# Optimization experiments

Hardware: AMD Instinct MI355X
Metric: run time of the kernel (lower is better)

Reference implementation:

```python
import jax, jax.numpy as jnp
import numpy as np

B = 16
N = [20000, 5000, 1250, 313, 79]          # node counts per pooling level (fine -> coarse)
E = [120000, 30000, 7500, 1878, 474]      # ~6 edges per node (triangle mesh)
FILTERS = [3, 32, 32, 64, 64, 64]
K = 6
Z = 64
COND = 2
N_LAYERS = 4


def setup_inputs():
    ks = iter(jax.random.split(jax.random.key(0), 64))
    inp = {}
    inp["x"] = jax.random.normal(next(ks), (B * N[0], FILTERS[0]), jnp.float32)
    inp["label"] = jax.random.normal(next(ks), (B, COND), jnp.float32)
    for i in range(5):
        inp[f"edges{i}"] = jax.random.randint(next(ks), (2, E[i]), 0, N[i])
    for i in range(4):
        inp[f"ds_idx{i}"] = jax.random.randint(next(ks), (N[i + 1],), 0, N[i])
        inp[f"us_idx{i}"] = jax.random.randint(next(ks), (N[i], 3), 0, N[i + 1])
        inp[f"us_w{i}"] = jax.random.uniform(next(ks), (N[i], 3), jnp.float32)
    for i in range(4):
        inp[f"enc_w{i}"] = 0.1 * jax.random.normal(next(ks), (K, FILTERS[i], FILTERS[i + 1]), jnp.float32)
        inp[f"enc_b{i}"] = 0.1 * jax.random.normal(next(ks), (FILTERS[i + 1],), jnp.float32)
    for i in range(5):
        inp[f"dec_w{i}"] = 0.1 * jax.random.normal(next(ks), (K, FILTERS[-i - 1], FILTERS[-i - 2]), jnp.float32)
    for i in range(4):
        inp[f"dec_b{i}"] = 0.1 * jax.random.normal(next(ks), (FILTERS[-i - 2],), jnp.float32)
    lat_in = N[4] * FILTERS[-1]
    inp["enc_mu_w"] = 0.1 * jax.random.normal(next(ks), (lat_in, Z), jnp.float32)
    inp["enc_mu_b"] = jnp.zeros((Z,), jnp.float32)
    inp["enc_lv_w"] = 0.1 * jax.random.normal(next(ks), (lat_in, Z), jnp.float32)
    inp["enc_lv_b"] = jnp.zeros((Z,), jnp.float32)
    inp["dec_lin_w"] = 0.1 * jax.random.normal(next(ks), (Z + COND, lat_in), jnp.float32)
    inp["dec_lin_b"] = jnp.zeros((lat_in,), jnp.float32)
    return inp


def _sym_norm(edges, n):
    # ChebConv_Coma.norm: norm = D^-1/2[row] * w * D^-1/2[col], unit weights
    row, col = edges[0], edges[1]
    deg = jnp.zeros((n,), jnp.float32).at[row].add(1.0)
    dinv = jnp.where(deg > 0, deg ** -0.5, 0.0)
    return dinv[row] * dinv[col]


def _cheb(x, edges, norm, W, b):
    # Chebyshev recursion: Tx_0=x, Tx_1=L~x, Tx_k=2 L~ Tx_{k-1} - Tx_{k-2}
    src, tgt = edges[0], edges[1]

    def prop(h):  # h: [B, Nn, F] -> scatter-sum of norm-weighted source features
        return jnp.zeros_like(h).at[:, tgt].add(h[:, src] * norm[None, :, None])

    Tx0 = x
    out = jnp.einsum('bnf,fg->bng', Tx0, W[0])
    Tx1 = prop(x)
    out = out + jnp.einsum('bnf,fg->bng', Tx1, W[1])
    for k in range(2, W.shape[0]):
        Tx2 = 2.0 * prop(Tx1) - Tx0
        out = out + jnp.einsum('bnf,fg->bng', Tx2, W[k])
        Tx0, Tx1 = Tx1, Tx2
    return out if b is None else out + b


def _forward(x, label, us_ws, enc_ws, enc_bs, dec_ws, dec_bs,
             enc_mu_w, enc_mu_b, enc_lv_w, enc_lv_b, dec_lin_w, dec_lin_b,
             edges, norms, ds_idx, us_idx):
    h = x.reshape(B, N[0], FILTERS[0])
    # encoder
    for i in range(N_LAYERS):
        h = jax.nn.relu(_cheb(h, edges[i], norms[i], enc_ws[i], enc_bs[i]))
        h = h[:, ds_idx[i]]  # binary downsample matrix == row gather
    h = h.reshape(B, N[4] * FILTERS[-1])
    mu = h @ enc_mu_w + enc_mu_b
    logvar = h @ enc_lv_w + enc_lv_b
    # reparameterize (fixed eps for determinism)
    eps = jax.random.normal(jax.random.key(42), mu.shape, mu.dtype)
    z = mu + eps * jnp.exp(0.5 * logvar)
    # decoder
    h = jnp.concatenate([z, label], axis=1)
    h = jax.nn.relu(h @ dec_lin_w + dec_lin_b).reshape(B, N[4], FILTERS[-1])
    for i in range(N_LAYERS):
        lvl = N_LAYERS - 1 - i
        # barycentric upsample: 3 nonzeros per output row
        h = jnp.einsum('rk,brkf->brf', us_ws[lvl], h[:, us_idx[lvl]])
        h = jax.nn.relu(_cheb(h, edges[lvl], norms[lvl], dec_ws[i], dec_bs[i]))
    # faithful quirk of the original: final conv uses A_edge_index[-1] (coarsest graph edges)
    h = _cheb(h, edges[-1], norms[-1], dec_ws[4], None)
    return h.reshape(-1, FILTERS[0]), mu, logvar


def reference(x, label,
              edges0, edges1, edges2, edges3, edges4,
              ds_idx0, ds_idx1, ds_idx2, ds_idx3,
              us_idx0, us_idx1, us_idx2, us_idx3,
              us_w0, us_w1, us_w2, us_w3,
              enc_w0, enc_w1, enc_w2, enc_w3,
              enc_b0, enc_b1, enc_b2, enc_b3,
              dec_w0, dec_w1, dec_w2, dec_w3, dec_w4,
              dec_b0, dec_b1, dec_b2, dec_b3,
              enc_mu_w, enc_mu_b, enc_lv_w, enc_lv_b, dec_lin_w, dec_lin_b):
    edges = [edges0, edges1, edges2, edges3, edges4]
    norms = [_sym_norm(edges[i], N[i]) for i in range(5)]
    return _forward(x, label,
                    [us_w0, us_w1, us_w2, us_w3],
                    [enc_w0, enc_w1, enc_w2, enc_w3],
                    [enc_b0, enc_b1, enc_b2, enc_b3],
                    [dec_w0, dec_w1, dec_w2, dec_w3, dec_w4],
                    [dec_b0, dec_b1, dec_b2, dec_b3],
                    enc_mu_w, enc_mu_b, enc_lv_w, enc_lv_b, dec_lin_w, dec_lin_b,
                    edges, norms,
                    [ds_idx0, ds_idx1, ds_idx2, ds_idx3],
                    [us_idx0, us_idx1, us_idx2, us_idx3])
```

## Files before the change

### kernel.cpp

```cpp
#include <hip/hip_runtime.h>
#include <cstdint>
#include <cstddef>

#define WG 256
#define NB 16


struct IP5 { const int* e[5]; };
struct Ptr3 { const float* p[3]; };


__global__ void k_zero_i(int* __restrict__ p, int n) {
  int i = blockIdx.x * WG + threadIdx.x;
  if (i < n) p[i] = 0;
}

__global__ void k_hist_all(IP5 ep, int* __restrict__ dsrc, int* __restrict__ dtgt) {
  int i = blockIdx.x * WG + threadIdx.x;
  if (i >= 159852) return;
  int l, eo, ee, no, co;
  if (i < 120000)      { l = 0; eo = 0;      ee = 120000; no = 0;     co = 0; }
  else if (i < 150000) { l = 1; eo = 120000; ee = 30000;  no = 20000; co = 20000; }
  else if (i < 157500) { l = 2; eo = 150000; ee = 7500;   no = 25000; co = 25000; }
  else if (i < 159378) { l = 3; eo = 157500; ee = 1878;   no = 26250; co = 26250; }
  else                 { l = 4; eo = 159378; ee = 474;    no = 26563; co = 26563; }
  int e = i - eo;
  const int* E = ep.e[l];
  atomicAdd(&dsrc[no + E[e]], 1);
  atomicAdd(&dtgt[co + E[ee + e]], 1);
}

__global__ void k_scan_all(const int* __restrict__ deg_all, int* __restrict__ rowptr_all,
                           int* __restrict__ cursor_all) {
  static const int Ns[5] = {20000, 5000, 1250, 313, 20000};
  static const int CO[5] = {0, 20000, 25000, 26250, 26563};
  static const int RO[5] = {0, 20001, 25002, 26253, 26567};
  __shared__ int s[WG];
  int l = blockIdx.x;
  int N = Ns[l];
  const int* deg = deg_all + CO[l];
  int* rowptr = rowptr_all + RO[l];
  int* cursor = cursor_all + CO[l];
  int t = threadIdx.x;
  int chunk = (N + WG - 1) / WG;
  int a = t * chunk;
  int b = min(N, a + chunk);
  int sum = 0;
  for (int i = a; i < b; i++) sum += deg[i];
  s[t] = sum;
  __syncthreads();
  for (int off = 1; off < WG; off <<= 1) {
    int v = (t >= off) ? s[t - off] : 0;
    __syncthreads();
    s[t] += v;
    __syncthreads();
  }
  int run = (t == 0) ? 0 : s[t - 1];
  for (int i = a; i < b; i++) {
    rowptr[i] = run;
    cursor[i] = run;
    run += deg[i];
  }
  if (t == 0) rowptr[N] = s[WG - 1];
}


static __device__ __forceinline__ float erfinv_f(float x) {
  float w = -log1pf(-x * x);
  float p;
  if (w < 5.0f) {
    w -= 2.5f;
    p = 2.81022636e-08f;
    p = fmaf(p, w, 3.43273939e-07f);
    p = fmaf(p, w, -3.5233877e-06f);
    p = fmaf(p, w, -4.39150654e-06f);
    p = fmaf(p, w, 0.00021858087f);
    p = fmaf(p, w, -0.00125372503f);
    p = fmaf(p, w, -0.00417768164f);
    p = fmaf(p, w, 0.246640727f);
    p = fmaf(p, w, 1.50140941f);
  } else {
    w = sqrtf(w) - 3.0f;
    p = -0.000200214257f;
    p = fmaf(p, w, 0.000100950558f);
    p = fmaf(p, w, 0.00134934322f);
    p = fmaf(p, w, -0.00367342844f);
    p = fmaf(p, w, 0.00573950773f);
    p = fmaf(p, w, -0.0076224613f);
    p = fmaf(p, w, 0.00943887047f);
    p = fmaf(p, w, 1.00167406f);
    p = fmaf(p, w, 2.83297682f);
  }
  return p * x;
}

static __device__ __forceinline__ float bits_to_normal(unsigned b) {
  float f = __uint_as_float((b >> 9) | 0x3f800000u) - 1.0f;
  const float lo = -0.99999994f;
  float u = f * (1.0f - lo) + lo;
  u = fmaxf(u, lo);
  return 1.41421356f * erfinv_f(u);
}

static __device__ __forceinline__ float eps_val(int i) {
  unsigned x0 = 0u, x1 = (unsigned)i;
  unsigned ks[3] = {0u, 42u, 0u ^ 42u ^ 0x1BD11BDAu};
  x0 += ks[0];
  x1 += ks[1];
  const int R[2][4] = {{13, 15, 26, 6}, {17, 29, 16, 24}};
#pragma unroll
  for (int it = 0; it < 5; it++) {
#pragma unroll
    for (int j = 0; j < 4; j++) {
      x0 += x1;
      int r = R[it & 1][j];
      x1 = (x1 << r) | (x1 >> (32 - r));
      x1 ^= x0;
    }
    x0 += ks[(it + 1) % 3];
    x1 += ks[(it + 2) % 3] + (unsigned)(it + 1);
  }
  return bits_to_normal(x0 ^ x1);
}

__global__ void k_fill_all(IP5 ep, const int* __restrict__ dsrc, int* __restrict__ cursor,
                           int* __restrict__ csrc, float* __restrict__ csw,
                           float* __restrict__ eps, const float* __restrict__ x,
                           float* __restrict__ sxl) {
  int blk = blockIdx.x;
  if (blk < 625) {
    int i = blk * WG + threadIdx.x;
    if (i >= 159852) return;
    int l, eo, ee, no, co, eb;
    if (i < 120000)      { l = 0; eo = 0;      ee = 120000; no = 0;     co = 0;     eb = 0; }
    else if (i < 150000) { l = 1; eo = 120000; ee = 30000;  no = 20000; co = 20000; eb = 120000; }
    else if (i < 157500) { l = 2; eo = 150000; ee = 7500;   no = 25000; co = 25000; eb = 150000; }
    else if (i < 159378) { l = 3; eo = 157500; ee = 1878;   no = 26250; co = 26250; eb = 157500; }
    else                 { l = 4; eo = 159378; ee = 474;    no = 26563; co = 26563; eb = 159378; }
    int e = i - eo;
    const int* E = ep.e[l];
    int s = E[e], t = E[ee + e];
    float da = (float)dsrc[no + s], db = (float)dsrc[no + t];
    float wa = (da > 0.f) ? (1.0f / sqrtf(da)) : 0.f;
    float wb = (db > 0.f) ? (1.0f / sqrtf(db)) : 0.f;
    int pos = atomicAdd(&cursor[co + t], 1);
    csrc[eb + pos] = s;
    csw[eb + pos] = wa * wb;
  } else if (blk < 629) {
    int j = (blk - 625) * WG + threadIdx.x;
    if (j < 1024) eps[j] = eps_val(j);
  } else {
    int j = (blk - 629) * WG + threadIdx.x;
    if (j >= NB * 20000 * 3) return;
    int f = j % 3;
    int b = (j / 3) % NB;
    int n = j / 48;
    sxl[j] = x[((size_t)b * 20000 + n) * 3 + f];
  }
}


#define RFL_I(v) __builtin_amdgcn_readfirstlane(v)
#define RFL_F(v) __int_as_float(__builtin_amdgcn_readfirstlane(__float_as_int(v)))

template <int F>
__global__ __launch_bounds__(WG) void k_propw(const float* __restrict__ in,
                                              float* __restrict__ out,
                                              const float* __restrict__ sub, float scale,
                                              const int* __restrict__ rowptr,
                                              const int* __restrict__ csrc,
                                              const float* __restrict__ csw, int N) {
  constexpr int C4 = F / 16;
  int node = blockIdx.x * 4 + (threadIdx.x >> 6);
  if (node >= N) return;
  int lane = threadIdx.x & 63;
  const float4* in4 = (const float4*)in;
  float4 acc[C4];
#pragma unroll
  for (int u = 0; u < C4; u++) acc[u] = make_float4(0.f, 0.f, 0.f, 0.f);
  int beg = rowptr[node], end = rowptr[node + 1];
  int j = beg;
  for (; j + 3 < end; j += 4) {
    int s0 = RFL_I(csrc[j]);
    int s1 = RFL_I(csrc[j + 1]);
    int s2 = RFL_I(csrc[j + 2]);
    int s3 = RFL_I(csrc[j + 3]);
    float w0 = RFL_F(csw[j]);
    float w1 = RFL_F(csw[j + 1]);
    float w2 = RFL_F(csw[j + 2]);
    float w3 = RFL_F(csw[j + 3]);
    const float4* p0 = in4 + (size_t)s0 * (4 * F) + lane;
    const float4* p1 = in4 + (size_t)s1 * (4 * F) + lane;
    const float4* p2 = in4 + (size_t)s2 * (4 * F) + lane;
    const float4* p3 = in4 + (size_t)s3 * (4 * F) + lane;
    float4 v0[C4], v1[C4], v2[C4], v3[C4];
#pragma unroll
    for (int u = 0; u < C4; u++) v0[u] = p0[u * 64];
#pragma unroll
    for (int u = 0; u < C4; u++) v1[u] = p1[u * 64];
#pragma unroll
    for (int u = 0; u < C4; u++) v2[u] = p2[u * 64];
#pragma unroll
    for (int u = 0; u < C4; u++) v3[u] = p3[u * 64];
#pragma unroll
    for (int u = 0; u < C4; u++) {
      acc[u].x = fmaf(w0, v0[u].x, acc[u].x); acc[u].y = fmaf(w0, v0[u].y, acc[u].y);
      acc[u].z = fmaf(w0, v0[u].z, acc[u].z); acc[u].w = fmaf(w0, v0[u].w, acc[u].w);
      acc[u].x = fmaf(w1, v1[u].x, acc[u].x); acc[u].y = fmaf(w1, v1[u].y, acc[u].y);
      acc[u].z = fmaf(w1, v1[u].z, acc[u].z); acc[u].w = fmaf(w1, v1[u].w, acc[u].w);
      acc[u].x = fmaf(w2, v2[u].x, acc[u].x); acc[u].y = fmaf(w2, v2[u].y, acc[u].y);
      acc[u].z = fmaf(w2, v2[u].z, acc[u].z); acc[u].w = fmaf(w2, v2[u].w, acc[u].w);
      acc[u].x = fmaf(w3, v3[u].x, acc[u].x); acc[u].y = fmaf(w3, v3[u].y, acc[u].y);
      acc[u].z = fmaf(w3, v3[u].z, acc[u].z); acc[u].w = fmaf(w3, v3[u].w, acc[u].w);
    }
  }
  for (; j < end; j++) {
    int s0 = RFL_I(csrc[j]);
    float w0 = RFL_F(csw[j]);
    const float4* p0 = in4 + (size_t)s0 * (4 * F) + lane;
#pragma unroll
    for (int u = 0; u < C4; u++) {
      float4 v0 = p0[u * 64];
      acc[u].x = fmaf(w0, v0.x, acc[u].x); acc[u].y = fmaf(w0, v0.y, acc[u].y);
      acc[u].z = fmaf(w0, v0.z, acc[u].z); acc[u].w = fmaf(w0, v0.w, acc[u].w);
    }
  }
  float4* o4 = (float4*)out + (size_t)node * (4 * F) + lane;
  if (sub) {
    const float4* s4 = (const float4*)sub + (size_t)node * (4 * F) + lane;
#pragma unroll
    for (int u = 0; u < C4; u++) {
      float4 sv = s4[u * 64];
      float4 r;
      r.x = fmaf(scale, acc[u].x, -sv.x); r.y = fmaf(scale, acc[u].y, -sv.y);
      r.z = fmaf(scale, acc[u].z, -sv.z); r.w = fmaf(scale, acc[u].w, -sv.w);
      o4[u * 64] = r;
    }
  } else {
#pragma unroll
    for (int u = 0; u < C4; u++) {
      float4 r;
      r.x = scale * acc[u].x; r.y = scale * acc[u].y;
      r.z = scale * acc[u].z; r.w = scale * acc[u].w;
      o4[u * 64] = r;
    }
  }
}

__global__ __launch_bounds__(WG) void k_propw3(const float* __restrict__ in,
                                               float* __restrict__ out,
                                               const float* __restrict__ sub, float scale,
                                               const int* __restrict__ rowptr,
                                               const int* __restrict__ csrc,
                                               const float* __restrict__ csw, int N) {
  int node = blockIdx.x * 4 + (threadIdx.x >> 6);
  if (node >= N) return;
  int lane = threadIdx.x & 63;
  if (lane >= 48) return;
  float acc = 0.f;
  int beg = rowptr[node], end = rowptr[node + 1];
  for (int j = beg; j < end; j++) {
    int s = RFL_I(csrc[j]);
    float w = RFL_F(csw[j]);
    acc = fmaf(w, in[(size_t)s * 48 + lane], acc);
  }
  float r = scale * acc;
  if (sub) r -= sub[(size_t)node * 48 + lane];
  out[(size_t)node * 48 + lane] = r;
}


template <int F, int G>
__global__ __launch_bounds__(WG) void k_gemm3(Ptr3 txs, const float* __restrict__ W,
                                              const float* __restrict__ bias,
                                              float* __restrict__ out, int rows,
                                              const int* __restrict__ idx,
                                              int accum, int relu) {
  constexpr int CG = G / 4;
  constexpr int RT = WG / CG;
  constexpr int RPB = RT * 4;
  __shared__ float sW[3 * F * G];
  for (int i = threadIdx.x; i < 3 * F * G; i += WG) sW[i] = W[i];
  __syncthreads();
  int cg = threadIdx.x % CG;
  int rt = threadIdx.x / CG;
  int row0 = blockIdx.x * RPB + rt * 4;
  if (row0 >= rows) return;
  size_t src0 = row0;
  if (idx) {
    int node = row0 >> 4, b = row0 & 15;
    src0 = (size_t)idx[node] * 16 + b;
  }
  float* o = out + (size_t)row0 * G + cg * 4;
  float4 acc[4];
  if (accum) {
#pragma unroll
    for (int r = 0; r < 4; r++) acc[r] = *(const float4*)(o + (size_t)r * G);
  } else if (bias) {
    float4 bv = *(const float4*)(bias + cg * 4);
#pragma unroll
    for (int r = 0; r < 4; r++) acc[r] = bv;
  } else {
#pragma unroll
    for (int r = 0; r < 4; r++) acc[r] = make_float4(0.f, 0.f, 0.f, 0.f);
  }
#pragma unroll
  for (int kk = 0; kk < 3; kk++) {
    const float* tb = txs.p[kk] + src0 * F;
    const float* w = sW + kk * F * G + cg * 4;
    if constexpr (F == 3) {
      float4 w0 = *(const float4*)(w + 0 * G);
      float4 w1 = *(const float4*)(w + 1 * G);
      float4 w2 = *(const float4*)(w + 2 * G);
#pragma unroll
      for (int r = 0; r < 4; r++) {
        float x0 = tb[r * 3 + 0], x1 = tb[r * 3 + 1], x2 = tb[r * 3 + 2];
        acc[r].x = fmaf(x0, w0.x, acc[r].x); acc[r].y = fmaf(x0, w0.y, acc[r].y);
        acc[r].z = fmaf(x0, w0.z, acc[r].z); acc[r].w = fmaf(x0, w0.w, acc[r].w);
        acc[r].x = fmaf(x1, w1.x, acc[r].x); acc[r].y = fmaf(x1, w1.y, acc[r].y);
        acc[r].z = fmaf(x1, w1.z, acc[r].z); acc[r].w = fmaf(x1, w1.w, acc[r].w);
        acc[r].x = fmaf(x2, w2.x, acc[r].x); acc[r].y = fmaf(x2, w2.y, acc[r].y);
        acc[r].z = fmaf(x2, w2.z, acc[r].z); acc[r].w = fmaf(x2, w2.w, acc[r].w);
      }
    } else {
#pragma unroll
      for (int fg = 0; fg < F / 4; fg++) {
        float4 xv[4];
#pragma unroll
        for (int r = 0; r < 4; r++) xv[r] = *(const float4*)(tb + (size_t)r * F + 4 * fg);
        float4 w0 = *(const float4*)(w + (4 * fg + 0) * G);
        float4 w1 = *(const float4*)(w + (4 * fg + 1) * G);
        float4 w2 = *(const float4*)(w + (4 * fg + 2) * G);
        float4 w3 = *(const float4*)(w + (4 * fg + 3) * G);
#pragma unroll
        for (int r = 0; r < 4; r++) {
          acc[r].x = fmaf(xv[r].x, w0.x, acc[r].x); acc[r].y = fmaf(xv[r].x, w0.y, acc[r].y);
          acc[r].z = fmaf(xv[r].x, w0.z, acc[r].z); acc[r].w = fmaf(xv[r].x, w0.w, acc[r].w);
          acc[r].x = fmaf(xv[r].y, w1.x, acc[r].x); acc[r].y = fmaf(xv[r].y, w1.y, acc[r].y);
          acc[r].z = fmaf(xv[r].y, w1.z, acc[r].z); acc[r].w = fmaf(xv[r].y, w1.w, acc[r].w);
          acc[r].x = fmaf(xv[r].z, w2.x, acc[r].x); acc[r].y = fmaf(xv[r].z, w2.y, acc[r].y);
          acc[r].z = fmaf(xv[r].z, w2.z, acc[r].z); acc[r].w = fmaf(xv[r].z, w2.w, acc[r].w);
          acc[r].x = fmaf(xv[r].w, w3.x, acc[r].x); acc[r].y = fmaf(xv[r].w, w3.y, acc[r].y);
          acc[r].z = fmaf(xv[r].w, w3.z, acc[r].z); acc[r].w = fmaf(xv[r].w, w3.w, acc[r].w);
        }
      }
    }
  }
  if (relu) {
#pragma unroll
    for (int r = 0; r < 4; r++) {
      acc[r].x = fmaxf(acc[r].x, 0.f); acc[r].y = fmaxf(acc[r].y, 0.f);
      acc[r].z = fmaxf(acc[r].z, 0.f); acc[r].w = fmaxf(acc[r].w, 0.f);
    }
  }
#pragma unroll
  for (int r = 0; r < 4; r++) *(float4*)(o + (size_t)r * G) = acc[r];
}

__global__ __launch_bounds__(WG) void k_gemm3_final(Ptr3 txs, const float* __restrict__ W,
                                                    const float* __restrict__ W4,
                                                    float* __restrict__ out,
                                                    float* __restrict__ dout, int rows) {
  constexpr int F = 32, G = 32;
  constexpr int CG = 8, RT = 32, RPB = 128;
  __shared__ float sW[3 * F * G];
  __shared__ float sWc[96];
  for (int i = threadIdx.x; i < 3 * F * G; i += WG) sW[i] = W[i];
  if (threadIdx.x < 96)
    sWc[threadIdx.x] = W4[threadIdx.x] - W4[192 + threadIdx.x] + W4[384 + threadIdx.x];
  __syncthreads();
  int cg = threadIdx.x % CG;
  int rt = threadIdx.x / CG;
  int row0 = blockIdx.x * RPB + rt * 4;
  float* o = out + (size_t)row0 * G + cg * 4;
  float4 acc[4];
#pragma unroll
  for (int r = 0; r < 4; r++) acc[r] = *(const float4*)(o + (size_t)r * G);
#pragma unroll
  for (int kk = 0; kk < 3; kk++) {
    const float* tb = txs.p[kk] + (size_t)row0 * F;
    const float* w = sW + kk * F * G + cg * 4;
#pragma unroll
    for (int fg = 0; fg < F / 4; fg++) {
      float4 xv[4];
#pragma unroll
      for (int r = 0; r < 4; r++) xv[r] = *(const float4*)(tb + (size_t)r * F + 4 * fg);
      float4 w0 = *(const float4*)(w + (4 * fg + 0) * G);
      float4 w1 = *(const float4*)(w + (4 * fg + 1) * G);
      float4 w2 = *(const float4*)(w + (4 * fg + 2) * G);
      float4 w3 = *(const float4*)(w + (4 * fg + 3) * G);
#pragma unroll
      for (int r = 0; r < 4; r++) {
        acc[r].x = fmaf(xv[r].x, w0.x, acc[r].x); acc[r].y = fmaf(xv[r].x, w0.y, acc[r].y);
        acc[r].z = fmaf(xv[r].x, w0.z, acc[r].z); acc[r].w = fmaf(xv[r].x, w0.w, acc[r].w);
        acc[r].x = fmaf(xv[r].y, w1.x, acc[r].x); acc[r].y = fmaf(xv[r].y, w1.y, acc[r].y);
        acc[r].z = fmaf(xv[r].y, w1.z, acc[r].z); acc[r].w = fmaf(xv[r].y, w1.w, acc[r].w);
        acc[r].x = fmaf(xv[r].z, w2.x, acc[r].x); acc[r].y = fmaf(xv[r].z, w2.y, acc[r].y);
        acc[r].z = fmaf(xv[r].z, w2.z, acc[r].z); acc[r].w = fmaf(xv[r].z, w2.w, acc[r].w);
        acc[r].x = fmaf(xv[r].w, w3.x, acc[r].x); acc[r].y = fmaf(xv[r].w, w3.y, acc[r].y);
        acc[r].z = fmaf(xv[r].w, w3.z, acc[r].z); acc[r].w = fmaf(xv[r].w, w3.w, acc[r].w);
      }
    }
  }
#pragma unroll
  for (int r = 0; r < 4; r++) {
    acc[r].x = fmaxf(acc[r].x, 0.f); acc[r].y = fmaxf(acc[r].y, 0.f);
    acc[r].z = fmaxf(acc[r].z, 0.f); acc[r].w = fmaxf(acc[r].w, 0.f);
  }
  if ((row0 >> 4) < 79) {
#pragma unroll
    for (int r = 0; r < 4; r++) *(float4*)(o + (size_t)r * G) = acc[r];
  }
#pragma unroll
  for (int r = 0; r < 4; r++) {
    float av[4] = {acc[r].x, acc[r].y, acc[r].z, acc[r].w};
    float p0 = 0.f, p1 = 0.f, p2 = 0.f;
#pragma unroll
    for (int j = 0; j < 4; j++) {
      int f = cg * 4 + j;
      p0 = fmaf(av[j], sWc[f * 3 + 0], p0);
      p1 = fmaf(av[j], sWc[f * 3 + 1], p1);
      p2 = fmaf(av[j], sWc[f * 3 + 2], p2);
    }
#pragma unroll
    for (int m = 4; m >= 1; m >>= 1) {
      p0 += __shfl_xor(p0, m, 64);
      p1 += __shfl_xor(p1, m, 64);
      p2 += __shfl_xor(p2, m, 64);
    }
    if (cg == 0) {
      int row = row0 + r;
      int n = row >> 4, b = row & 15;
      float* od = dout + ((size_t)b * 20000 + n) * 3;
      od[0] = p0; od[1] = p1; od[2] = p2;
    }
  }
}

__global__ __launch_bounds__(256) void k_final_fix(const float* __restrict__ in,
                                                   const float* __restrict__ W,
                                                   const int* __restrict__ rowptr,
                                                   const int* __restrict__ csrc,
                                                   const float* __restrict__ csw,
                                                   float* __restrict__ out) {
  __shared__ float B0[79 * 32], B1[79 * 32], B2[79 * 32];
  __shared__ float sacc[79 * 3];
  __shared__ float sW[576];
  int b = blockIdx.x, t = threadIdx.x;
  for (int i = t; i < 576; i += 256) sW[i] = W[i];
  for (int i = t; i < 2528; i += 256) {
    int r = i >> 5, f = i & 31;
    B0[i] = in[((size_t)r * 16 + b) * 32 + f];
  }
  __syncthreads();
  for (int i = t; i < 237; i += 256) {
    int r = i / 3, g = i % 3;
    float a = 0.f;
    for (int f = 0; f < 32; f++) a = fmaf(B0[r * 32 + f], sW[f * 3 + g], a);
    sacc[i] = a;
  }
  for (int i = t; i < 2528; i += 256) {
    int r = i >> 5, f = i & 31;
    float a = 0.f;
    for (int j = rowptr[r]; j < rowptr[r + 1]; j++) a = fmaf(csw[j], B0[csrc[j] * 32 + f], a);
    B1[i] = a;
  }
  __syncthreads();
  for (int i = t; i < 237; i += 256) {
    int r = i / 3, g = i % 3;
    float a = sacc[i];
    for (int f = 0; f < 32; f++) a = fmaf(B1[r * 32 + f], sW[96 + f * 3 + g], a);
    sacc[i] = a;
  }
  for (int i = t; i < 2528; i += 256) {
    int r = i >> 5, f = i & 31;
    float a = 0.f;
    for (int j = rowptr[r]; j < rowptr[r + 1]; j++) a = fmaf(csw[j], B1[csrc[j] * 32 + f], a);
    B2[i] = 2.f * a - B0[i];
  }
  __syncthreads();
  for (int i = t; i < 237; i += 256) {
    int r = i / 3, g = i % 3;
    float a = sacc[i];
    for (int f = 0; f < 32; f++) a = fmaf(B2[r * 32 + f], sW[192 + f * 3 + g], a);
    sacc[i] = a;
  }
  __syncthreads();
  for (int i = t; i < 2528; i += 256) {
    int r = i >> 5, f = i & 31;
    float a = 0.f;
    for (int j = rowptr[r]; j < rowptr[r + 1]; j++) a = fmaf(csw[j], B2[csrc[j] * 32 + f], a);
    B0[i] = 2.f * a - B1[i];
  }
  __syncthreads();
  for (int i = t; i < 237; i += 256) {
    int r = i / 3, g = i % 3;
    float a = sacc[i];
    for (int f = 0; f < 32; f++) a = fmaf(B0[r * 32 + f], sW[288 + f * 3 + g], a);
    sacc[i] = a;
  }
  __syncthreads();
  for (int i = t; i < 2528; i += 256) {
    int r = i >> 5, f = i & 31;
    float a = 0.f;
    for (int j = rowptr[r]; j < rowptr[r + 1]; j++) a = fmaf(csw[j], B0[csrc[j] * 32 + f], a);
    B1[i] = 2.f * a - B2[i];
  }
  __syncthreads();
  for (int i = t; i < 237; i += 256) {
    int r = i / 3, g = i % 3;
    float a = sacc[i];
    for (int f = 0; f < 32; f++) a = fmaf(B1[r * 32 + f], sW[384 + f * 3 + g], a);
    sacc[i] = a;
  }
  __syncthreads();
  for (int i = t; i < 2528; i += 256) {
    int r = i >> 5, f = i & 31;
    float a = 0.f;
    for (int j = rowptr[r]; j < rowptr[r + 1]; j++) a = fmaf(csw[j], B1[csrc[j] * 32 + f], a);
    B2[i] = 2.f * a - B0[i];
  }
  __syncthreads();
  for (int i = t; i < 237; i += 256) {
    int r = i / 3, g = i % 3;
    float a = sacc[i];
    for (int f = 0; f < 32; f++) a = fmaf(B2[r * 32 + f], sW[480 + f * 3 + g], a);
    out[((size_t)b * 20000 + r) * 3 + g] = a;
  }
}

template <int F>
__global__ __launch_bounds__(WG) void k_us(const float* __restrict__ in,
                                           float* __restrict__ out,
                                           const int* __restrict__ uidx,
                                           const float* __restrict__ uw, int Nf) {
  int i = blockIdx.x * WG + threadIdx.x;
  int total = Nf * NB * F;
  if (i >= total) return;
  int pos = i % (NB * F);
  int r = i / (NB * F);
  float acc = 0.f;
#pragma unroll
  for (int k = 0; k < 3; k++) {
    float v = in[(size_t)uidx[r * 3 + k] * NB * F + pos];
    acc = fmaf(uw[r * 3 + k], fmaxf(v, 0.f), acc);
  }
  out[i] = acc;
}


__global__ __launch_bounds__(64) void k_latent(const float* __restrict__ h,
                                               const float* __restrict__ muW,
                                               const float* __restrict__ muB,
                                               const float* __restrict__ lvW,
                                               const float* __restrict__ lvB,
                                               const float* __restrict__ eps,
                                               const float* __restrict__ label,
                                               float* __restrict__ mu_out,
                                               float* __restrict__ lv_out,
                                               float* __restrict__ hcat) {
  int b = blockIdx.x / 64;
  int g = blockIdx.x % 64;
  int l = threadIdx.x;
  float am = 0.f, al = 0.f;
  for (int i = l; i < 5056; i += 64) {
    int n = i >> 6, f = i & 63;
    float hv = h[(size_t)(n * 16 + b) * 64 + f];
    am = fmaf(hv, muW[(size_t)i * 64 + g], am);
    al = fmaf(hv, lvW[(size_t)i * 64 + g], al);
  }
  for (int off = 32; off > 0; off >>= 1) {
    am += __shfl_down(am, off, 64);
    al += __shfl_down(al, off, 64);
  }
  if (l == 0) {
    am += muB[g];
    al += lvB[g];
    mu_out[b * 64 + g] = am;
    lv_out[b * 64 + g] = al;
    hcat[b * 66 + g] = fmaf(eps[b * 64 + g], expf(0.5f * al), am);
    if (g < 2) hcat[b * 66 + 64 + g] = label[b * 2 + g];
  }
}

__global__ __launch_bounds__(WG) void k_declin(const float* __restrict__ hcat,
                                               const float* __restrict__ W,
                                               const float* __restrict__ bias,
                                               float* __restrict__ out) {
  int idx = blockIdx.x * WG + threadIdx.x;
  if (idx >= NB * 5056) return;
  int b = idx / 5056, j = idx % 5056;
  int n = j >> 6, f = j & 63;
  float acc = bias[j];
  const float* hc = hcat + b * 66;
#pragma unroll
  for (int i = 0; i < 66; i++) acc = fmaf(hc[i], W[(size_t)i * 5056 + j], acc);
  out[(size_t)(n * 16 + b) * 64 + f] = fmaxf(acc, 0.f);
}


static inline dim3 grid1(long n) { return dim3((unsigned)((n + WG - 1) / WG)); }

template <int F, int G>
static void run_cheb(float* in, float* out, float* A, float* B,
                     const float* W, const float* bias, int N, int Nout,
                     const int* ds_idx, int relu_last,
                     const int* rowptr, const int* csrc, const float* csw,
                     hipStream_t st) {
  int orows = NB * Nout;
  constexpr int RPB = (WG / (G / 4)) * 4;
  dim3 gG((unsigned)((orows + RPB - 1) / RPB));
  dim3 gP((unsigned)((N + 3) / 4));
  int relu2 = ds_idx ? 1 : relu_last;
  if constexpr (F == 3) {
    k_propw3<<<gP, WG, 0, st>>>(in, A, nullptr, 1.f, rowptr, csrc, csw, N);
    k_propw3<<<gP, WG, 0, st>>>(A, B, in, 2.f, rowptr, csrc, csw, N);
    Ptr3 p1{{in, A, B}};
    k_gemm3<F, G><<<gG, WG, 0, st>>>(p1, W, bias, out, orows, ds_idx, 0, 0);
    k_propw3<<<gP, WG, 0, st>>>(B, in, A, 2.f, rowptr, csrc, csw, N);
    k_propw3<<<gP, WG, 0, st>>>(in, A, B, 2.f, rowptr, csrc, csw, N);
    k_propw3<<<gP, WG, 0, st>>>(A, B, in, 2.f, rowptr, csrc, csw, N);
    Ptr3 p2{{in, A, B}};
    k_gemm3<F, G><<<gG, WG, 0, st>>>(p2, W + 3 * F * G, nullptr, out, orows, ds_idx, 1, relu2);
  } else {
    k_propw<F><<<gP, WG, 0, st>>>(in, A, nullptr, 1.f, rowptr, csrc, csw, N);
    k_propw<F><<<gP, WG, 0, st>>>(A, B, in, 2.f, rowptr, csrc, csw, N);
    Ptr3 p1{{in, A, B}};
    k_gemm3<F, G><<<gG, WG, 0, st>>>(p1, W, bias, out, orows, ds_idx, 0, 0);
    k_propw<F><<<gP, WG, 0, st>>>(B, in, A, 2.f, rowptr, csrc, csw, N);
    k_propw<F><<<gP, WG, 0, st>>>(in, A, B, 2.f, rowptr, csrc, csw, N);
    k_propw<F><<<gP, WG, 0, st>>>(A, B, in, 2.f, rowptr, csrc, csw, N);
    Ptr3 p2{{in, A, B}};
    k_gemm3<F, G><<<gG, WG, 0, st>>>(p2, W + 3 * F * G, nullptr, out, orows, ds_idx, 1, relu2);
  }
}

extern "C" void kernel_launch(void* const* d_in, const int* in_sizes, int n_in,
                              void* d_out, int out_size, void* d_ws, size_t ws_size,
                              hipStream_t stream) {
  const float* x = (const float*)d_in[0];
  const float* label = (const float*)d_in[1];
  IP5 ep;
  for (int l = 0; l < 5; l++) ep.e[l] = (const int*)d_in[2 + l];
  const int* ds_idx[4];
  const int* us_idx[4];
  const float* us_w[4];
  for (int i = 0; i < 4; i++) {
    ds_idx[i] = (const int*)d_in[7 + 3 * i];
    us_idx[i] = (const int*)d_in[8 + 3 * i];
    us_w[i] = (const float*)d_in[9 + 3 * i];
  }
  const float* enc_w[4];
  const float* enc_b[4];
  for (int i = 0; i < 4; i++) {
    enc_w[i] = (const float*)d_in[19 + 2 * i];
    enc_b[i] = (const float*)d_in[20 + 2 * i];
  }
  const float* dec_w[5];
  for (int i = 0; i < 5; i++) dec_w[i] = (const float*)d_in[27 + i];
  const float* dec_b[4];
  for (int i = 0; i < 4; i++) dec_b[i] = (const float*)d_in[32 + i];
  const float* mu_w = (const float*)d_in[36];
  const float* mu_b = (const float*)d_in[37];
  const float* lv_w = (const float*)d_in[38];
  const float* lv_b = (const float*)d_in[39];
  const float* dl_w = (const float*)d_in[40];
  const float* dl_b = (const float*)d_in[41];

  float* wsf = (float*)d_ws;
  size_t off = 0;
  auto carve = [&](size_t n) -> float* {
    float* p = wsf + off;
    off += (n + 63) & ~(size_t)63;
    return p;
  };
  const size_t SLOT = 10240000;
  float* s0 = carve(SLOT);
  float* s1 = carve(SLOT);
  float* s2 = carve(SLOT);
  float* s3 = carve(SLOT);
  float* sxl = carve(960000);
  int* deg_all = (int*)carve(26642 + 46563);
  int* deg_src_all = deg_all;
  int* deg_tgt_all = deg_all + 26642;
  int* rowptr_all = (int*)carve(46568);
  int* cursor_all = (int*)carve(46563);
  int* csrc_all = (int*)carve(159852);
  float* csw_all = carve(159852);
  float* eps = carve(1024);
  float* hcat = carve(1056);

  static const int ROFF[5] = {0, 20001, 25002, 26253, 26567};
  static const int EOFF[5] = {0, 120000, 150000, 157500, 159378};
  auto RP = [&](int l) { return rowptr_all + ROFF[l]; };
  auto CS = [&](int l) { return csrc_all + EOFF[l]; };
  auto CW = [&](int l) { return csw_all + EOFF[l]; };

  k_zero_i<<<grid1(26642 + 46563), WG, 0, stream>>>(deg_all, 26642 + 46563);
  k_hist_all<<<grid1(159852), WG, 0, stream>>>(ep, deg_src_all, deg_tgt_all);
  k_scan_all<<<5, WG, 0, stream>>>(deg_tgt_all, rowptr_all, cursor_all);
  k_fill_all<<<625 + 4 + 3750, WG, 0, stream>>>(ep, deg_src_all, cursor_all, csrc_all,
                                                csw_all, eps, x, sxl);

  float* mu_out = (float*)d_out + 960000;
  float* lv_out = (float*)d_out + 961024;

  run_cheb<3, 32>(sxl, s1, s2, s3, enc_w[0], enc_b[0], 20000, 5000, ds_idx[0], 0,
                  RP(0), CS(0), CW(0), stream);
  run_cheb<32, 32>(s1, s0, s2, s3, enc_w[1], enc_b[1], 5000, 1250, ds_idx[1], 0,
                   RP(1), CS(1), CW(1), stream);
  run_cheb<32, 64>(s0, s1, s2, s3, enc_w[2], enc_b[2], 1250, 313, ds_idx[2], 0,
                   RP(2), CS(2), CW(2), stream);
  run_cheb<64, 64>(s1, s0, s2, s3, enc_w[3], enc_b[3], 313, 79, ds_idx[3], 0,
                   RP(3), CS(3), CW(3), stream);

  k_latent<<<1024, 64, 0, stream>>>(s0, mu_w, mu_b, lv_w, lv_b, eps, label, mu_out, lv_out, hcat);
  k_declin<<<grid1(NB * 5056), WG, 0, stream>>>(hcat, dl_w, dl_b, s0);

  k_us<64><<<grid1((long)313 * NB * 64), WG, 0, stream>>>(s0, s1, us_idx[3], us_w[3], 313);
  run_cheb<64, 64>(s1, s0, s2, s3, dec_w[0], dec_b[0], 313, 313, nullptr, 0,
                   RP(3), CS(3), CW(3), stream);
  k_us<64><<<grid1((long)1250 * NB * 64), WG, 0, stream>>>(s0, s1, us_idx[2], us_w[2], 1250);
  run_cheb<64, 64>(s1, s0, s2, s3, dec_w[1], dec_b[1], 1250, 1250, nullptr, 0,
                   RP(2), CS(2), CW(2), stream);
  k_us<64><<<grid1((long)5000 * NB * 64), WG, 0, stream>>>(s0, s1, us_idx[1], us_w[1], 5000);
  run_cheb<64, 32>(s1, s0, s2, s3, dec_w[2], dec_b[2], 5000, 5000, nullptr, 0,
                   RP(1), CS(1), CW(1), stream);
  k_us<32><<<grid1((long)20000 * NB * 32), WG, 0, stream>>>(s0, s1, us_idx[0], us_w[0], 20000);

  {
    const int N = 20000;
    int rows = NB * N;
    dim3 gP((unsigned)((N + 3) / 4));
    dim3 gG((unsigned)(rows / 128));
    k_propw<32><<<gP, WG, 0, stream>>>(s1, s2, nullptr, 1.f, RP(0), CS(0), CW(0), N);
    k_propw<32><<<gP, WG, 0, stream>>>(s2, s3, s1, 2.f, RP(0), CS(0), CW(0), N);
    Ptr3 p1{{s1, s2, s3}};
    dim3 gG1((unsigned)(rows / 128));
    k_gemm3<32, 32><<<gG1, WG, 0, stream>>>(p1, dec_w[3], dec_b[3], s0, rows, nullptr, 0, 0);
    k_propw<32><<<gP, WG, 0, stream>>>(s3, s1, s2, 2.f, RP(0), CS(0), CW(0), N);
    k_propw<32><<<gP, WG, 0, stream>>>(s1, s2, s3, 2.f, RP(0), CS(0), CW(0), N);
    k_propw<32><<<gP, WG, 0, stream>>>(s2, s3, s1, 2.f, RP(0), CS(0), CW(0), N);
    Ptr3 p2{{s1, s2, s3}};
    k_gemm3_final<<<gG, WG, 0, stream>>>(p2, dec_w[3] + 3 * 32 * 32, dec_w[4], s0,
                                         (float*)d_out, rows);
  }

  k_final_fix<<<16, 256, 0, stream>>>(s0, dec_w[4], RP(4), CS(4), CW(4), (float*)d_out);
}
```

Before: 1.333 ms.

## Stage GEMM input rows through LDS for 32-wide Chebyshev output GEMMs

Adds new GEMM kernels for the 32-output-channel Chebyshev layers and the final decoder layer. They cooperatively load a tile of input rows into padded shared memory with coalesced reads, then each thread computes 4 rows by 8 output columns. Previously each thread read strided float4 rows straight from global memory. The intent is better coalescing and more register reuse of weights, at the cost of extra LDS traffic and barriers per Chebyshev term. The final kernel shrinks its cross-lane reduction from 8 lanes to 4.

```diff
diff --git a/kernel.cpp b/kernel.cpp
--- a/kernel.cpp
+++ b/kernel.cpp
@@ -8,6 +8,11 @@
 
 struct IP5 { const int* e[5]; };
 struct Ptr3 { const float* p[3]; };
+
+static __device__ __forceinline__ void fma4(float4& a, float s, const float4& b) {
+  a.x = fmaf(s, b.x, a.x); a.y = fmaf(s, b.y, a.y);
+  a.z = fmaf(s, b.z, a.z); a.w = fmaf(s, b.w, a.w);
+}
 
 
 __global__ void k_zero_i(int* __restrict__ p, int n) {
@@ -204,14 +209,10 @@
     for (int u = 0; u < C4; u++) v3[u] = p3[u * 64];
 #pragma unroll
     for (int u = 0; u < C4; u++) {
-      acc[u].x = fmaf(w0, v0[u].x, acc[u].x); acc[u].y = fmaf(w0, v0[u].y, acc[u].y);
-      acc[u].z = fmaf(w0, v0[u].z, acc[u].z); acc[u].w = fmaf(w0, v0[u].w, acc[u].w);
-      acc[u].x = fmaf(w1, v1[u].x, acc[u].x); acc[u].y = fmaf(w1, v1[u].y, acc[u].y);
-      acc[u].z = fmaf(w1, v1[u].z, acc[u].z); acc[u].w = fmaf(w1, v1[u].w, acc[u].w);
-      acc[u].x = fmaf(w2, v2[u].x, acc[u].x); acc[u].y = fmaf(w2, v2[u].y, acc[u].y);
-      acc[u].z = fmaf(w2, v2[u].z, acc[u].z); acc[u].w = fmaf(w2, v2[u].w, acc[u].w);
-      acc[u].x = fmaf(w3, v3[u].x, acc[u].x); acc[u].y = fmaf(w3, v3[u].y, acc[u].y);
-      acc[u].z = fmaf(w3, v3[u].z, acc[u].z); acc[u].w = fmaf(w3, v3[u].w, acc[u].w);
+      fma4(acc[u], w0, v0[u]);
+      fma4(acc[u], w1, v1[u]);
+      fma4(acc[u], w2, v2[u]);
+      fma4(acc[u], w3, v3[u]);
     }
   }
   for (; j < end; j++) {
@@ -221,8 +222,7 @@
 #pragma unroll
     for (int u = 0; u < C4; u++) {
       float4 v0 = p0[u * 64];
-      acc[u].x = fmaf(w0, v0.x, acc[u].x); acc[u].y = fmaf(w0, v0.y, acc[u].y);
-      acc[u].z = fmaf(w0, v0.z, acc[u].z); acc[u].w = fmaf(w0, v0.w, acc[u].w);
+      fma4(acc[u], w0, v0);
     }
   }
   float4* o4 = (float4*)out + (size_t)node * (4 * F) + lane;
@@ -270,6 +270,200 @@
 }
 
 
+template <int F, int BS>
+__global__ __launch_bounds__(BS) void k_gemm3s(Ptr3 txs, const float* __restrict__ W,
+                                               const float* __restrict__ bias,
+                                               float* __restrict__ out, int rows,
+                                               const int* __restrict__ idx,
+                                               int accum, int relu) {
+  constexpr int PF = F + 4;
+  constexpr int RPB = BS;
+  __shared__ float sX[RPB * PF];
+  __shared__ float sW[3 * F * 32];
+  int tid = threadIdx.x;
+  for (int i = tid; i < 3 * F * 32; i += BS) sW[i] = W[i];
+  int row0 = blockIdx.x * RPB;
+  int cg = tid & 3;
+  int lr0 = (tid >> 6) * 64 + ((tid >> 2) & 15);
+  float4 acc[4][2];
+  if (accum) {
+#pragma unroll
+    for (int r = 0; r < 4; r++) {
+      int gr = row0 + lr0 + 16 * r;
+      if (gr < rows) {
+        const float* o = out + (size_t)gr * 32 + cg * 8;
+        acc[r][0] = *(const float4*)o;
+        acc[r][1] = *(const float4*)(o + 4);
+      } else {
+        acc[r][0] = acc[r][1] = make_float4(0.f, 0.f, 0.f, 0.f);
+      }
+    }
+  } else if (bias) {
+    float4 b0 = *(const float4*)(bias + cg * 8);
+    float4 b1 = *(const float4*)(bias + cg * 8 + 4);
+#pragma unroll
+    for (int r = 0; r < 4; r++) { acc[r][0] = b0; acc[r][1] = b1; }
+  } else {
+#pragma unroll
+    for (int r = 0; r < 4; r++)
+      acc[r][0] = acc[r][1] = make_float4(0.f, 0.f, 0.f, 0.f);
+  }
+  for (int kk = 0; kk < 3; kk++) {
+    __syncthreads();
+    const float* src = txs.p[kk];
+    if (idx) {
+      int node0 = row0 >> 4;
+      for (int i = tid; i < RPB * F; i += BS) {
+        int nl = i / (16 * F);
+        int off = i - nl * (16 * F);
+        int ng = node0 + nl;
+        float v = 0.f;
+        if (ng * 16 < rows) v = src[(size_t)idx[ng] * (16 * F) + off];
+        int rr = i / F;
+        sX[rr * PF + (i - rr * F)] = v;
+      }
+    } else {
+      for (int i = tid; i < RPB * F; i += BS) {
+        float v = 0.f;
+        long g = (long)row0 * F + i;
+        if (g < (long)rows * F) v = src[g];
+        int rr = i / F;
+        sX[rr * PF + (i - rr * F)] = v;
+      }
+    }
+    __syncthreads();
+    const float* wk = sW + kk * F * 32;
+#pragma unroll
+    for (int fg = 0; fg < F / 4; fg++) {
+      float4 wA[4][2];
+#pragma unroll
+      for (int f = 0; f < 4; f++) {
+        wA[f][0] = *(const float4*)(wk + (4 * fg + f) * 32 + cg * 8);
+        wA[f][1] = *(const float4*)(wk + (4 * fg + f) * 32 + cg * 8 + 4);
+      }
+#pragma unroll
+      for (int r = 0; r < 4; r++) {
+        float4 xv = *(const float4*)(sX + (lr0 + 16 * r) * PF + 4 * fg);
+        fma4(acc[r][0], xv.x, wA[0][0]); fma4(acc[r][1], xv.x, wA[0][1]);
+        fma4(acc[r][0], xv.y, wA[1][0]); fma4(acc[r][1], xv.y, wA[1][1]);
+        fma4(acc[r][0], xv.z, wA[2][0]); fma4(acc[r][1], xv.z, wA[2][1]);
+        fma4(acc[r][0], xv.w, wA[3][0]); fma4(acc[r][1], xv.w, wA[3][1]);
+      }
+    }
+  }
+  if (relu) {
+#pragma unroll
+    for (int r = 0; r < 4; r++) {
+      acc[r][0].x = fmaxf(acc[r][0].x, 0.f); acc[r][0].y = fmaxf(acc[r][0].y, 0.f);
+      acc[r][0].z = fmaxf(acc[r][0].z, 0.f); acc[r][0].w = fmaxf(acc[r][0].w, 0.f);
+      acc[r][1].x = fmaxf(acc[r][1].x, 0.f); acc[r][1].y = fmaxf(acc[r][1].y, 0.f);
+      acc[r][1].z = fmaxf(acc[r][1].z, 0.f); acc[r][1].w = fmaxf(acc[r][1].w, 0.f);
+    }
+  }
+#pragma unroll
+  for (int r = 0; r < 4; r++) {
+    int gr = row0 + lr0 + 16 * r;
+    if (gr < rows) {
+      float* o = out + (size_t)gr * 32 + cg * 8;
+      *(float4*)o = acc[r][0];
+      *(float4*)(o + 4) = acc[r][1];
+    }
+  }
+}
+
+__global__ __launch_bounds__(256) void k_gemm3s_final(Ptr3 txs, const float* __restrict__ W,
+                                                      const float* __restrict__ W4,
+                                                      float* __restrict__ out,
+                                                      float* __restrict__ dout, int rows) {
+  constexpr int F = 32, PF = 36, RPB = 256, BS = 256;
+  __shared__ float sX[RPB * PF];
+  __shared__ float sW[3 * F * 32];
+  __shared__ float sWc[96];
+  int tid = threadIdx.x;
+  for (int i = tid; i < 3 * F * 32; i += BS) sW[i] = W[i];
+  if (tid < 96) sWc[tid] = W4[tid] - W4[192 + tid] + W4[384 + tid];
+  int row0 = blockIdx.x * RPB;
+  int cg = tid & 3;
+  int lr0 = (tid >> 6) * 64 + ((tid >> 2) & 15);
+  float4 acc[4][2];
+#pragma unroll
+  for (int r = 0; r < 4; r++) {
+    const float* o = out + (size_t)(row0 + lr0 + 16 * r) * 32 + cg * 8;
+    acc[r][0] = *(const float4*)o;
+    acc[r][1] = *(const float4*)(o + 4);
+  }
+  for (int kk = 0; kk < 3; kk++) {
+    __syncthreads();
+    const float* src = txs.p[kk] + (size_t)row0 * F;
+    for (int i = tid; i < RPB * F; i += BS) {
+      int rr = i / F;
+      sX[rr * PF + (i - rr * F)] = src[i];
+    }
+    __syncthreads();
+    const float* wk = sW + kk * F * 32;
+#pragma unroll
+    for (int fg = 0; fg < F / 4; fg++) {
+      float4 wA[4][2];
+#pragma unroll
+      for (int f = 0; f < 4; f++) {
+        wA[f][0] = *(const float4*)(wk + (4 * fg + f) * 32 + cg * 8);
+        wA[f][1] = *(const float4*)(wk + (4 * fg + f) * 32 + cg * 8 + 4);
+      }
+#pragma unroll
+      for (int r = 0; r < 4; r++) {
+        float4 xv = *(const float4*)(sX + (lr0 + 16 * r) * PF + 4 * fg);
+        fma4(acc[r][0], xv.x, wA[0][0]); fma4(acc[r][1], xv.x, wA[0][1]);
+        fma4(acc[r][0], xv.y, wA[1][0]); fma4(acc[r][1], xv.y, wA[1][1]);
+        fma4(acc[r][0], xv.z, wA[2][0]); fma4(acc[r][1], xv.z, wA[2][1]);
+        fma4(acc[r][0], xv.w, wA[3][0]); fma4(acc[r][1], xv.w, wA[3][1]);
+      }
+    }
+  }
+#pragma unroll
+  for (int r = 0; r < 4; r++) {
+    acc[r][0].x = fmaxf(acc[r][0].x, 0.f); acc[r][0].y = fmaxf(acc[r][0].y, 0.f);
+    acc[r][0].z = fmaxf(acc[r][0].z, 0.f); acc[r][0].w = fmaxf(acc[r][0].w, 0.f);
+    acc[r][1].x = fmaxf(acc[r][1].x, 0.f); acc[r][1].y = fmaxf(acc[r][1].y, 0.f);
+    acc[r][1].z = fmaxf(acc[r][1].z, 0.f); acc[r][1].w = fmaxf(acc[r][1].w, 0.f);
+  }
+#pragma unroll
+  for (int r = 0; r < 4; r++) {
+    int gr = row0 + lr0 + 16 * r;
+    if ((gr >> 4) < 79) {
+      float* o = out + (size_t)gr * 32 + cg * 8;
+      *(float4*)o = acc[r][0];
+      *(float4*)(o + 4) = acc[r][1];
+    }
+  }
+  float wc[8][3];
+#pragma unroll
+  for (int j = 0; j < 8; j++) {
+    int f = cg * 8 + j;
+    wc[j][0] = sWc[f * 3 + 0]; wc[j][1] = sWc[f * 3 + 1]; wc[j][2] = sWc[f * 3 + 2];
+  }
+#pragma unroll
+  for (int r = 0; r < 4; r++) {
+    float av[8] = {acc[r][0].x, acc[r][0].y, acc[r][0].z, acc[r][0].w,
+                   acc[r][1].x, acc[r][1].y, acc[r][1].z, acc[r][1].w};
+    float p0 = 0.f, p1 = 0.f, p2 = 0.f;
+#pragma unroll
+    for (int j = 0; j < 8; j++) {
+      p0 = fmaf(av[j], wc[j][0], p0);
+      p1 = fmaf(av[j], wc[j][1], p1);
+      p2 = fmaf(av[j], wc[j][2], p2);
+    }
+    p0 += __shfl_xor(p0, 1, 64); p1 += __shfl_xor(p1, 1, 64); p2 += __shfl_xor(p2, 1, 64);
+    p0 += __shfl_xor(p0, 2, 64); p1 += __shfl_xor(p1, 2, 64); p2 += __shfl_xor(p2, 2, 64);
+    if (cg == 0) {
+      int row = row0 + lr0 + 16 * r;
+      int n = row >> 4, b = row & 15;
+      float* od = dout + ((size_t)b * 20000 + n) * 3;
+      od[0] = p0; od[1] = p1; od[2] = p2;
+    }
+  }
+}
+
+
 template <int F, int G>
 __global__ __launch_bounds__(WG) void k_gemm3(Ptr3 txs, const float* __restrict__ W,
                                               const float* __restrict__ bias,
@@ -315,12 +509,9 @@
 #pragma unroll
       for (int r = 0; r < 4; r++) {
         float x0 = tb[r * 3 + 0], x1 = tb[r * 3 + 1], x2 = tb[r * 3 + 2];
-        acc[r].x = fmaf(x0, w0.x, acc[r].x); acc[r].y = fmaf(x0, w0.y, acc[r].y);
-        acc[r].z = fmaf(x0, w0.z, acc[r].z); acc[r].w = fmaf(x0, w0.w, acc[r].w);
-        acc[r].x = fmaf(x1, w1.x, acc[r].x); acc[r].y = fmaf(x1, w1.y, acc[r].y);
-        acc[r].z = fmaf(x1, w1.z, acc[r].z); acc[r].w = fmaf(x1, w1.w, acc[r].w);
-        acc[r].x = fmaf(x2, w2.x, acc[r].x); acc[r].y = fmaf(x2, w2.y, acc[r].y);
-        acc[r].z = fmaf(x2, w2.z, acc[r].z); acc[r].w = fmaf(x2, w2.w, acc[r].w);
+        fma4(acc[r], x0, w0);
+        fma4(acc[r], x1, w1);
+        fma4(acc[r], x2, w2);
       }
     } else {
 #pragma unroll
@@ -334,14 +525,10 @@
         float4 w3 = *(const float4*)(w + (4 * fg + 3) * G);
 #pragma unroll
         for (int r = 0; r < 4; r++) {
-          acc[r].x = fmaf(xv[r].x, w0.x, acc[r].x); acc[r].y = fmaf(xv[r].x, w0.y, acc[r].y);
-          acc[r].z = fmaf(xv[r].x, w0.z, acc[r].z); acc[r].w = fmaf(xv[r].x, w0.w, acc[r].w);
-          acc[r].x = fmaf(xv[r].y, w1.x, acc[r].x); acc[r].y = fmaf(xv[r].y, w1.y, acc[r].y);
-          acc[r].z = fmaf(xv[r].y, w1.z, acc[r].z); acc[r].w = fmaf(xv[r].y, w1.w, acc[r].w);
-          acc[r].x = fmaf(xv[r].z, w2.x, acc[r].x); acc[r].y = fmaf(xv[r].z, w2.y, acc[r].y);
-          acc[r].z = fmaf(xv[r].z, w2.z, acc[r].z); acc[r].w = fmaf(xv[r].z, w2.w, acc[r].w);
-          acc[r].x = fmaf(xv[r].w, w3.x, acc[r].x); acc[r].y = fmaf(xv[r].w, w3.y, acc[r].y);
-          acc[r].z = fmaf(xv[r].w, w3.z, acc[r].z); acc[r].w = fmaf(xv[r].w, w3.w, acc[r].w);
+          fma4(acc[r], xv[r].x, w0);
+          fma4(acc[r], xv[r].y, w1);
+          fma4(acc[r], xv[r].z, w2);
+          fma4(acc[r], xv[r].w, w3);
         }
       }
     }
@@ -355,86 +542,6 @@
   }
 #pragma unroll
   for (int r = 0; r < 4; r++) *(float4*)(o + (size_t)r * G) = acc[r];
-}
-
-__global__ __launch_bounds__(WG) void k_gemm3_final(Ptr3 txs, const float* __restrict__ W,
-                                                    const float* __restrict__ W4,
-                                                    float* __restrict__ out,
-                                                    float* __restrict__ dout, int rows) {
-  constexpr int F = 32, G = 32;
-  constexpr int CG = 8, RT = 32, RPB = 128;
-  __shared__ float sW[3 * F * G];
-  __shared__ float sWc[96];
-  for (int i = threadIdx.x; i < 3 * F * G; i += WG) sW[i] = W[i];
-  if (threadIdx.x < 96)
-    sWc[threadIdx.x] = W4[threadIdx.x] - W4[192 + threadIdx.x] + W4[384 + threadIdx.x];
-  __syncthreads();
-  int cg = threadIdx.x % CG;
-  int rt = threadIdx.x / CG;
-  int row0 = blockIdx.x * RPB + rt * 4;
-  float* o = out + (size_t)row0 * G + cg * 4;
-  float4 acc[4];
-#pragma unroll
-  for (int r = 0; r < 4; r++) acc[r] = *(const float4*)(o + (size_t)r * G);
-#pragma unroll
-  for (int kk = 0; kk < 3; kk++) {
-    const float* tb = txs.p[kk] + (size_t)row0 * F;
-    const float* w = sW + kk * F * G + cg * 4;
-#pragma unroll
-    for (int fg = 0; fg < F / 4; fg++) {
-      float4 xv[4];
-#pragma unroll
-      for (int r = 0; r < 4; r++) xv[r] = *(const float4*)(tb + (size_t)r * F + 4 * fg);
-      float4 w0 = *(const float4*)(w + (4 * fg + 0) * G);
-      float4 w1 = *(const float4*)(w + (4 * fg + 1) * G);
-      float4 w2 = *(const float4*)(w + (4 * fg + 2) * G);
-      float4 w3 = *(const float4*)(w + (4 * fg + 3) * G);
-#pragma unroll
-      for (int r = 0; r < 4; r++) {
-        acc[r].x = fmaf(xv[r].x, w0.x, acc[r].x); acc[r].y = fmaf(xv[r].x, w0.y, acc[r].y);
-        acc[r].z = fmaf(xv[r].x, w0.z, acc[r].z); acc[r].w = fmaf(xv[r].x, w0.w, acc[r].w);
-        acc[r].x = fmaf(xv[r].y, w1.x, acc[r].x); acc[r].y = fmaf(xv[r].y, w1.y, acc[r].y);
-        acc[r].z = fmaf(xv[r].y, w1.z, acc[r].z); acc[r].w = fmaf(xv[r].y, w1.w, acc[r].w);
-        acc[r].x = fmaf(xv[r].z, w2.x, acc[r].x); acc[r].y = fmaf(xv[r].z, w2.y, acc[r].y);
-        acc[r].z = fmaf(xv[r].z, w2.z, acc[r].z); acc[r].w = fmaf(xv[r].z, w2.w, acc[r].w);
-        acc[r].x = fmaf(xv[r].w, w3.x, acc[r].x); acc[r].y = fmaf(xv[r].w, w3.y, acc[r].y);
-        acc[r].z = fmaf(xv[r].w, w3.z, acc[r].z); acc[r].w = fmaf(xv[r].w, w3.w, acc[r].w);
-      }
-    }
-  }
-#pragma unroll
-  for (int r = 0; r < 4; r++) {
-    acc[r].x = fmaxf(acc[r].x, 0.f); acc[r].y = fmaxf(acc[r].y, 0.f);
-    acc[r].z = fmaxf(acc[r].z, 0.f); acc[r].w = fmaxf(acc[r].w, 0.f);
-  }
-  if ((row0 >> 4) < 79) {
-#pragma unroll
-    for (int r = 0; r < 4; r++) *(float4*)(o + (size_t)r * G) = acc[r];
-  }
-#pragma unroll
-  for (int r = 0; r < 4; r++) {
-    float av[4] = {acc[r].x, acc[r].y, acc[r].z, acc[r].w};
-    float p0 = 0.f, p1 = 0.f, p2 = 0.f;
-#pragma unroll
-    for (int j = 0; j < 4; j++) {
-      int f = cg * 4 + j;
-      p0 = fmaf(av[j], sWc[f * 3 + 0], p0);
-      p1 = fmaf(av[j], sWc[f * 3 + 1], p1);
-      p2 = fmaf(av[j], sWc[f * 3 + 2], p2);
-    }
-#pragma unroll
-    for (int m = 4; m >= 1; m >>= 1) {
-      p0 += __shfl_xor(p0, m, 64);
-      p1 += __shfl_xor(p1, m, 64);
-      p2 += __shfl_xor(p2, m, 64);
-    }
-    if (cg == 0) {
-      int row = row0 + r;
-      int n = row >> 4, b = row & 15;
-      float* od = dout + ((size_t)b * 20000 + n) * 3;
-      od[0] = p0; od[1] = p1; od[2] = p2;
-    }
-  }
 }
 
 __global__ __launch_bounds__(256) void k_final_fix(const float* __restrict__ in,
@@ -608,11 +715,11 @@
                      const int* rowptr, const int* csrc, const float* csw,
                      hipStream_t st) {
   int orows = NB * Nout;
-  constexpr int RPB = (WG / (G / 4)) * 4;
-  dim3 gG((unsigned)((orows + RPB - 1) / RPB));
   dim3 gP((unsigned)((N + 3) / 4));
   int relu2 = ds_idx ? 1 : relu_last;
   if constexpr (F == 3) {
+    constexpr int RPB = (WG / (G / 4)) * 4;
+    dim3 gG((unsigned)((orows + RPB - 1) / RPB));
     k_propw3<<<gP, WG, 0, st>>>(in, A, nullptr, 1.f, rowptr, csrc, csw, N);
     k_propw3<<<gP, WG, 0, st>>>(A, B, in, 2.f, rowptr, csrc, csw, N);
     Ptr3 p1{{in, A, B}};
@@ -622,7 +729,21 @@
     k_propw3<<<gP, WG, 0, st>>>(A, B, in, 2.f, rowptr, csrc, csw, N);
     Ptr3 p2{{in, A, B}};
     k_gemm3<F, G><<<gG, WG, 0, st>>>(p2, W + 3 * F * G, nullptr, out, orows, ds_idx, 1, relu2);
+  } else if constexpr (G == 32) {
+    constexpr int BS = (F == 64) ? 128 : 256;
+    dim3 gG((unsigned)((orows + BS - 1) / BS));
+    k_propw<F><<<gP, WG, 0, st>>>(in, A, nullptr, 1.f, rowptr, csrc, csw, N);
+    k_propw<F><<<gP, WG, 0, st>>>(A, B, in, 2.f, rowptr, csrc, csw, N);
+    Ptr3 p1{{in, A, B}};
+    k_gemm3s<F, BS><<<gG, BS, 0, st>>>(p1, W, bias, out, orows, ds_idx, 0, 0);
+    k_propw<F><<<gP, WG, 0, st>>>(B, in, A, 2.f, rowptr, csrc, csw, N);
+    k_propw<F><<<gP, WG, 0, st>>>(in, A, B, 2.f, rowptr, csrc, csw, N);
+    k_propw<F><<<gP, WG, 0, st>>>(A, B, in, 2.f, rowptr, csrc, csw, N);
+    Ptr3 p2{{in, A, B}};
+    k_gemm3s<F, BS><<<gG, BS, 0, st>>>(p2, W + 3 * F * G, nullptr, out, orows, ds_idx, 1, relu2);
   } else {
+    constexpr int RPB = (WG / (G / 4)) * 4;
+    dim3 gG((unsigned)((orows + RPB - 1) / RPB));
     k_propw<F><<<gP, WG, 0, st>>>(in, A, nullptr, 1.f, rowptr, csrc, csw, N);
     k_propw<F><<<gP, WG, 0, st>>>(A, B, in, 2.f, rowptr, csrc, csw, N);
     Ptr3 p1{{in, A, B}};
@@ -732,18 +853,17 @@
     const int N = 20000;
     int rows = NB * N;
     dim3 gP((unsigned)((N + 3) / 4));
-    dim3 gG((unsigned)(rows / 128));
+    dim3 gG((unsigned)(rows / 256));
     k_propw<32><<<gP, WG, 0, stream>>>(s1, s2, nullptr, 1.f, RP(0), CS(0), CW(0), N);
     k_propw<32><<<gP, WG, 0, stream>>>(s2, s3, s1, 2.f, RP(0), CS(0), CW(0), N);
     Ptr3 p1{{s1, s2, s3}};
-    dim3 gG1((unsigned)(rows / 128));
-    k_gemm3<32, 32><<<gG1, WG, 0, stream>>>(p1, dec_w[3], dec_b[3], s0, rows, nullptr, 0, 0);
+    k_gemm3s<32, 256><<<gG, 256, 0, stream>>>(p1, dec_w[3], dec_b[3], s0, rows, nullptr, 0, 0);
     k_propw<32><<<gP, WG, 0, stream>>>(s3, s1, s2, 2.f, RP(0), CS(0), CW(0), N);
     k_propw<32><<<gP, WG, 0, stream>>>(s1, s2, s3, 2.f, RP(0), CS(0), CW(0), N);
     k_propw<32><<<gP, WG, 0, stream>>>(s2, s3, s1, 2.f, RP(0), CS(0), CW(0), N);
     Ptr3 p2{{s1, s2, s3}};
-    k_gemm3_final<<<gG, WG, 0, stream>>>(p2, dec_w[3] + 3 * 32 * 32, dec_w[4], s0,
-                                         (float*)d_out, rows);
+    k_gemm3s_final<<<gG, 256, 0, stream>>>(p2, dec_w[3] + 3 * 32 * 32, dec_w[4], s0,
+                                           (float*)d_out, rows);
   }
 
   k_final_fix<<<16, 256, 0, stream>>>(s0, dec_w[4], RP(4), CS(4), CW(4), (float*)d_out);
```

Result: slower. 1.606 ms (+20.4%).
